# Performance work log

Hardware: AMD Instinct MI355X
Metric: run time of the kernel (lower is better)

The kernel has to match this reference:

```python
import jax, jax.numpy as jnp
import numpy as np

# Scattering config (matches init_kwargs)
T = 16384       # input_shape
J = 8           # max_scale_power
Q = 8           # fo_wavelets (first-order wavelets per octave); Q2 = 1
B = 16          # batch
STRIDE = 2 ** J # final lowpass subsampling -> output length T // STRIDE = 64
XI_MAX = 0.35   # max normalized center frequency (standard Morlet choice)


def _build_filters():
    """Analytic Morlet-style filter bank, defined directly in frequency domain
    as Gaussians (positive-frequency support -> analytic wavelets)."""
    freqs = np.arange(T, dtype=np.float64) / T  # normalized freq grid [0,1)
    # First order: Q wavelets per octave over J octaves
    n1 = J * Q
    xi1 = XI_MAX * 2.0 ** (-np.arange(n1) / Q)
    sigma1 = xi1 * (2.0 ** (1.0 / Q) - 1.0)          # bandwidth ~ filter spacing
    psi1 = np.exp(-(freqs[None, :] - xi1[:, None]) ** 2 / (2.0 * sigma1[:, None] ** 2))
    # Second order: Q2=1 wavelet per octave
    xi2 = XI_MAX * 2.0 ** (-np.arange(J, dtype=np.float64))
    sigma2 = xi2 * 0.5
    psi2 = np.exp(-(freqs[None, :] - xi2[:, None]) ** 2 / (2.0 * sigma2[:, None] ** 2))
    # Lowpass phi: Gaussian at DC with cutoff ~ 2^-J (symmetric in freq)
    f_sym = np.minimum(freqs, 1.0 - freqs)
    sigma_phi = XI_MAX * 2.0 ** (-J)
    phi = np.exp(-f_sym ** 2 / (2.0 * sigma_phi ** 2))
    # Valid second-order paths: xi2[j2] < xi1[j1] (frequency-decreasing cascade)
    i1g, i2g = np.meshgrid(np.arange(n1), np.arange(J), indexing="ij")
    valid = xi2[i2g] < xi1[i1g]
    pair_j1 = i1g[valid].astype(np.int32)  # 224 pairs for J=8, Q=8
    pair_j2 = i2g[valid].astype(np.int32)
    return (psi1.astype(np.float32), psi2.astype(np.float32),
            phi.astype(np.float32), pair_j1, pair_j2)


def setup_inputs() -> dict:
    key = jax.random.key(0)
    x = jax.random.normal(key, (B, T), dtype=jnp.float32)
    psi1, psi2, phi, p1, p2 = _build_filters()
    return {
        "x": x,
        "psi1_hat": jnp.asarray(psi1),   # [n1, T]
        "psi2_hat": jnp.asarray(psi2),   # [n2, T]
        "phi_hat": jnp.asarray(phi),     # [T]
        "pair_j1": jnp.asarray(p1),      # [P] int32
        "pair_j2": jnp.asarray(p2),      # [P] int32
    }


def reference(x, psi1_hat, psi2_hat, phi_hat, pair_j1, pair_j2):
    """1D wavelet scattering: FFT-domain Morlet convs + complex modulus +
    lowpass + downsample by 2^J. Returns (order0, order1, order2) coefficients,
    mirroring WaveletScatter1d's per-order tuple."""
    xh = jnp.fft.fft(x)                                             # [B, T] complex
    # Order 0: S0 = subsample(x * phi)
    S0 = jnp.fft.ifft(xh * phi_hat).real[:, None, ::STRIDE]          # [B, 1, T/2^J]
    # Order 1: U1_j = |x * psi1_j|
    U1 = jnp.abs(jnp.fft.ifft(xh[:, None, :] * psi1_hat[None, :, :]))  # [B, n1, T]
    U1h = jnp.fft.fft(U1)                                            # [B, n1, T]
    S1 = jnp.fft.ifft(U1h * phi_hat).real[:, :, ::STRIDE]            # [B, n1, T/2^J]
    # Order 2: U2_{j1,j2} = ||x*psi1_j1| * psi2_j2| for valid pairs (xi2 < xi1)
    U2 = jnp.abs(jnp.fft.ifft(U1h[:, pair_j1, :] * psi2_hat[pair_j2][None]))  # [B, P, T]
    S2 = jnp.fft.ifft(jnp.fft.fft(U2) * phi_hat).real[:, :, ::STRIDE]         # [B, P, T/2^J]
    return (S0, S1, S2)
```

## Files before the change

kernel.cpp:

```cpp
#include <hip/hip_runtime.h>
#include <math.h>


#define T_N   16384
#define NT    512
#define NTS   256
#define B_SZ  16
#define N1    64
#define NPAIR 224
#define FOLD_F 256
#define USTRIDE 8208
#define INV_N (1.0f/16384.0f)
#define TWO_PI 6.283185307179586f

typedef float v2f __attribute__((ext_vector_type(2)));

__device__ __forceinline__ int pad(int i) { return i + (i >> 4); }

__device__ __forceinline__ v2f cmulw(v2f a, v2f w){
  v2f n; n.x = -a.y; n.y = a.x;
  return w.x * a + w.y * n;
}
__device__ __forceinline__ constexpr int br4(int x){
  return ((x&1)<<3)|((x&2)<<1)|((x&4)>>1)|((x&8)>>3);
}
template<int LB>
__device__ __forceinline__ constexpr int brN(int x){
  int r=0;
  for(int i=0;i<LB;++i){ r=(r<<1)|((x>>i)&1); }
  return r;
}
__device__ __forceinline__ int rev4_14(int p){
  unsigned r = __brev((unsigned)p) >> 18;
  return (int)(((r & 0x2AAAu) >> 1) | ((r & 0x1555u) << 1));
}

__device__ __forceinline__ void twiddle_tree(v2f w, v2f* tw){
  tw[0].x = 1.f; tw[0].y = 0.f;
  tw[1] = w;
  tw[2] = cmulw(w, w);
  tw[4] = cmulw(tw[2], tw[2]);
  tw[8] = cmulw(tw[4], tw[4]);
  tw[3] = cmulw(tw[2], w);
  tw[5] = cmulw(tw[4], w);
  tw[6] = cmulw(tw[4], tw[2]);
  tw[7] = cmulw(tw[4], tw[3]);
  tw[9]  = cmulw(tw[8], w);
  tw[10] = cmulw(tw[8], tw[2]);
  tw[11] = cmulw(tw[8], tw[3]);
  tw[12] = cmulw(tw[8], tw[4]);
  tw[13] = cmulw(tw[8], tw[5]);
  tw[14] = cmulw(tw[8], tw[6]);
  tw[15] = cmulw(tw[8], tw[7]);
}

template<int SGN, int LOGNN>
__device__ __forceinline__ void dft_reg(v2f* a){
  constexpr int NN = 1<<LOGNN;
  static constexpr float C16[16] = {
    1.f, 0.98078528f, 0.92387953f, 0.83146961f, 0.70710678f, 0.55557023f,
    0.38268343f, 0.19509032f, 0.f, -0.19509032f, -0.38268343f, -0.55557023f,
    -0.70710678f, -0.83146961f, -0.92387953f, -0.98078528f };
  static constexpr float S16[16] = {
    0.f, 0.19509032f, 0.38268343f, 0.55557023f, 0.70710678f, 0.83146961f,
    0.92387953f, 0.98078528f, 1.f, 0.98078528f, 0.92387953f, 0.83146961f,
    0.70710678f, 0.55557023f, 0.38268343f, 0.19509032f };
#pragma unroll
  for (int m = NN/2; m >= 1; m >>= 1) {
#pragma unroll
    for (int base = 0; base < NN; base += 2*m) {
#pragma unroll
      for (int j = 0; j < m; ++j) {
        v2f u = a[base+j], v = a[base+j+m];
        a[base+j] = u + v;
        v2f w = u - v;
        const int ti = (j*16)/m;
        v2f tw; tw.x = C16[ti]; tw.y = (float)SGN * S16[ti];
        a[base+j+m] = cmulw(w, tw);
      }
    }
  }
}
template<int SGN>
__device__ __forceinline__ void dft16(v2f* a){ dft_reg<SGN,4>(a); }

template<int SGN, int M, int LOGM>
__device__ __forceinline__ void super_dif16(v2f* d, int g)
{
  const int j = g & (M-1);
  const int base = ((g >> LOGM) << (LOGM+4)) | j;
  v2f* dp = d + pad(base);
  v2f a[16];
#pragma unroll
  for (int k = 0; k < 16; ++k) a[k] = dp[k*M + ((k*M)>>4)];
  dft16<SGN>(a);
  float sj, cj;
  __sincosf((float)SGN * (TWO_PI / (16.f*(float)M)) * (float)j, &sj, &cj);
  v2f w; w.x = cj; w.y = sj;
  v2f tw[16];
  twiddle_tree(w, tw);
  dp[0] = a[0];
#pragma unroll
  for (int r = 1; r < 16; ++r)
    dp[r*M + ((r*M)>>4)] = cmulw(a[br4(r)], tw[r]);
}

template<int SGN, int M, int LOGM>
__device__ __forceinline__ void super_dif16_sp8(v2f* d, int g)
{
  static constexpr float CW[16] = { 1.f, 0.92387953f, 0.70710678f, 0.38268343f,
    0.f, -0.38268343f, -0.70710678f, -0.92387953f, -1.f, -0.92387953f,
    -0.70710678f, -0.38268343f, 0.f, 0.38268343f, 0.70710678f, 0.92387953f };
  static constexpr float SW[16] = { 0.f, 0.38268343f, 0.70710678f, 0.92387953f,
    1.f, 0.92387953f, 0.70710678f, 0.38268343f, 0.f, -0.38268343f,
    -0.70710678f, -0.92387953f, -1.f, -0.92387953f, -0.70710678f, -0.38268343f };
  const int j = g & (M-1);
  const int base = ((g >> LOGM) << (LOGM+4)) | j;
  v2f* dp = d + pad(base);
  v2f a[8];
#pragma unroll
  for (int m = 0; m < 8; ++m) a[m] = dp[m*M + ((m*M)>>4)];
  v2f y[16];
#pragma unroll
  for (int r0 = 0; r0 < 2; ++r0) {
    v2f z[8];
    z[0] = a[0];
#pragma unroll
    for (int m = 1; m < 8; ++m) {
      v2f w; w.x = CW[(m*r0)&15]; w.y = (float)SGN*SW[(m*r0)&15];
      z[m] = cmulw(a[m], w);
    }
    v2f E[4], O[4];
    {
      v2f e0=z[0]+z[4], e1=z[0]-z[4], o0=z[2]+z[6], o1=z[2]-z[6];
      v2f io; io.x=-(float)SGN*o1.y; io.y=(float)SGN*o1.x;
      E[0]=e0+o0; E[1]=e1+io; E[2]=e0-o0; E[3]=e1-io;
    }
    {
      v2f e0=z[1]+z[5], e1=z[1]-z[5], o0=z[3]+z[7], o1=z[3]-z[7];
      v2f io; io.x=-(float)SGN*o1.y; io.y=(float)SGN*o1.x;
      O[0]=e0+o0; O[1]=e1+io; O[2]=e0-o0; O[3]=e1-io;
    }
    constexpr float RT = 0.70710678f;
#pragma unroll
    for (int r1 = 0; r1 < 4; ++r1) {
      v2f w8;
      if (r1 == 0)      { w8.x = 1.f;  w8.y = 0.f; }
      else if (r1 == 1) { w8.x = RT;   w8.y = (float)SGN*RT; }
      else if (r1 == 2) { w8.x = 0.f;  w8.y = (float)SGN; }
      else              { w8.x = -RT;  w8.y = (float)SGN*RT; }
      v2f t = cmulw(O[r1], w8);
      y[2*r1 + r0]     = E[r1] + t;
      y[2*r1 + r0 + 8] = E[r1] - t;
    }
  }
  float sj, cj;
  __sincosf((float)SGN * (TWO_PI / (16.f*(float)M)) * (float)j, &sj, &cj);
  v2f w; w.x = cj; w.y = sj;
  v2f tw[16];
  twiddle_tree(w, tw);
  dp[0] = y[0];
#pragma unroll
  for (int r = 1; r < 16; ++r)
    dp[r*M + ((r*M)>>4)] = cmulw(y[r], tw[r]);
}

template<int SGN, int M, int LOGM>
__device__ __forceinline__ void super_dit16(v2f* d, int g)
{
  const int j = g & (M-1);
  const int base = ((g >> LOGM) << (LOGM+4)) | j;
  v2f* dp = d + pad(base);
  float sj, cj;
  __sincosf((float)SGN * (TWO_PI / (16.f*(float)M)) * (float)j, &sj, &cj);
  v2f w; w.x = cj; w.y = sj;
  v2f tw[16];
  twiddle_tree(w, tw);
  v2f a[16];
  a[0] = dp[0];
#pragma unroll
  for (int k = 1; k < 16; ++k)
    a[k] = cmulw(dp[k*M + ((k*M)>>4)], tw[k]);
  dft16<SGN>(a);
#pragma unroll
  for (int r = 0; r < 16; ++r) dp[r*M + ((r*M)>>4)] = a[br4(r)];
}

template<int SGN, int LOGM1, int RMAX, bool JLIM>
__device__ __forceinline__ void final_prune(v2f* ds, int t)
{
  static constexpr float CW[16] = { 1.f, 0.92387953f, 0.70710678f, 0.38268343f,
    0.f, -0.38268343f, -0.70710678f, -0.92387953f, -1.f, -0.92387953f,
    -0.70710678f, -0.38268343f, 0.f, 0.38268343f, 0.70710678f, 0.92387953f };
  static constexpr float SW[16] = { 0.f, 0.38268343f, 0.70710678f, 0.92387953f,
    1.f, 0.92387953f, 0.70710678f, 0.38268343f, 0.f, -0.38268343f,
    -0.70710678f, -0.92387953f, -1.f, -0.92387953f, -0.70710678f, -0.38268343f };
  constexpr int M1 = 1<<LOGM1;
  const int j = t;
  if (JLIM && j >= 256) return;
  v2f* dp = ds + j + (j>>4);
  float sj, cj;
  __sincosf((float)SGN * (TWO_PI / (16.f*(float)M1)) * (float)j, &sj, &cj);
  v2f w; w.x = cj; w.y = sj;
  v2f tw[16];
  twiddle_tree(w, tw);
  v2f b[16];
  b[0] = dp[0];
#pragma unroll
  for (int k = 1; k < 16; ++k)
    b[k] = cmulw(dp[k*M1 + ((k*M1)>>4)], tw[k]);
#pragma unroll
  for (int r = 0; r < RMAX; ++r) {
    v2f acc = b[0];
#pragma unroll
    for (int k = 1; k < 16; ++k) {
      v2f wc; wc.x = CW[(r*k)&15]; wc.y = (float)SGN*SW[(r*k)&15];
      acc += cmulw(b[k], wc);
    }
    dp[r*M1 + ((r*M1)>>4)] = acc;
  }
}

template<int SGN, int LOGM>
__device__ __forceinline__ void dif_chain(v2f* ds, int t){
  super_dif16<SGN, (1<<LOGM), LOGM>(ds, t);
  __syncthreads();
  if constexpr (LOGM > 4) dif_chain<SGN, LOGM-4>(ds, t);
}
template<int SGN, int LOGM, int LOGTOP>
__device__ __forceinline__ void dit_chain(v2f* ds, int t){
  super_dit16<SGN, (1<<LOGM), LOGM>(ds, t);
  __syncthreads();
  if constexpr (LOGM + 4 < LOGTOP) dit_chain<SGN, LOGM+4, LOGTOP>(ds, t);
}

template<int LOGMM>
__device__ __forceinline__ void mid_generic(v2f* ds, int t)
{
  constexpr int MM = 1<<LOGMM;
  v2f* dp = ds + 17*t;
#pragma unroll
  for (int q = 0; q < 16/MM; ++q) {
    v2f a[MM];
#pragma unroll
    for (int i = 0; i < MM; ++i) a[i] = dp[q*MM+i];
    dft_reg<+1,LOGMM>(a);
    v2f m[MM];
#pragma unroll
    for (int r = 0; r < MM; ++r) {
      v2f y = a[brN<LOGMM>(r)];
      m[r].x = INV_N * sqrtf(y.x*y.x + y.y*y.y);
      m[r].y = 0.f;
    }
    dft_reg<-1,LOGMM>(m);
#pragma unroll
    for (int k = 0; k < MM; ++k) dp[q*MM+k] = m[brN<LOGMM>(k)];
  }
}

template<int LOGN, int RMAX, bool JL, int K1ST>
__device__ __forceinline__ void o2_body(v2f* ds, int t)
{
  constexpr int LOGM1 = LOGN-4;
  if constexpr (K1ST == 16) super_dif16<+1, (1<<LOGM1), LOGM1>(ds, t);
  else                      super_dif16_sp8<+1, (1<<LOGM1), LOGM1>(ds, t);
  __syncthreads();
  dif_chain<+1, LOGM1-4>(ds, t);
  constexpr int LOGMM = ((LOGM1-5)%4)+1;
  mid_generic<LOGMM>(ds, t);
  __syncthreads();
  dit_chain<-1, LOGMM, LOGM1>(ds, t);
  final_prune<-1, LOGM1, RMAX, JL>(ds, t);
  __syncthreads();
}

template<int PERK>
__device__ __forceinline__ void fold_generic(const v2f* ds, const float* __restrict__ phi,
                                             float* outp, int t, float scale)
{
  const int k = t / PERK, g = t % PERK;
  float sv, cv, ss, cs;
  __sincosf((TWO_PI/64.f) * (float)((g*k) & 63), &sv, &cv);
  __sincosf((TWO_PI/64.f) * (float)((PERK*k) & 63), &ss, &cs);
  float acc = 0.f;
#pragma unroll
  for (int m = 0; m < 256/PERK; ++m) {
    const int f = g + PERK*m;
    v2f u = ds[f + (f>>4)];
    float wgt = phi[f] * ((f == 0) ? 1.f : 2.f);
    acc += wgt * (u.x*cv - u.y*sv);
    float nc = cv*cs - sv*ss, ns = cv*ss + sv*cs;
    cv = nc; sv = ns;
  }
#pragma unroll
  for (int o = 1; o < PERK; o <<= 1) acc += __shfl_xor(acc, o);
  if (g == 0) outp[k] = acc * scale;
}

__device__ __forceinline__ void fold32(v2f* ds, const float* __restrict__ phi,
                                       float* outp, int t, float scale, bool valid)
{
#pragma unroll
  for (int h = 0; h < 2; ++h) {
    const int g = t + 32*h;
    v2f acc; acc.x = 0.f; acc.y = 0.f;
#pragma unroll
    for (int m = 0; m < 4; ++m) {
      const int f = g + 64*m;
      v2f u = ds[f + (f>>4)];
      float wgt = phi[f] * ((f == 0) ? 1.f : 2.f);
      acc += wgt * u;
    }
    const int s = 384 + g;
    ds[s + (s>>4)] = acc;
  }
  __syncthreads();
  if (valid) {
#pragma unroll
    for (int h = 0; h < 2; ++h) {
      const int k = t + 32*h;
      float ss, cs;
      __sincosf((TWO_PI/64.f) * (float)k, &ss, &cs);
      float cv = 1.f, sv = 0.f, acc = 0.f;
      for (int g = 0; g < 64; ++g) {
        const int s = 384 + g;
        v2f V = ds[s + (s>>4)];
        acc += V.x*cv - V.y*sv;
        float nc = cv*cs - sv*ss, ns = cv*ss + sv*cs;
        cv = nc; sv = ns;
      }
      outp[k] = acc * scale;
    }
  }
}

__device__ __forceinline__ int pair_index(int j1, int j2)
{
  const int q = j1 >> 3;
  return 8*(7*q - (q*(q-1))/2) + (j1 & 7)*(7 - q) + (j2 - q - 1);
}

__device__ __constant__ int WTAB[8]  = {16384, 12903, 6452, 3226, 1613, 807, 404, 202};
__device__ __constant__ int TBTAB[8] = {4600, 2300, 1152, 576, 292, 148, 76, 40};

__device__ __forceinline__ float2 f2add(float2 a, float2 b){ return make_float2(a.x+b.x, a.y+b.y); }
__device__ __forceinline__ float2 f2sub(float2 a, float2 b){ return make_float2(a.x-b.x, a.y-b.y); }
__device__ __forceinline__ float2 cmul_cs(float2 a, float c, float s){
  return make_float2(a.x*c - a.y*s, a.x*s + a.y*c);
}
__device__ void dif_sweep(float2* d, int tid, float sgn, int mb_hi, int mb_lo)
{
  const float ang = sgn * (TWO_PI / (float)T_N);
  for (int mbits = mb_hi; mbits >= mb_lo; mbits -= 2) {
    const int M = 1 << mbits;
#pragma unroll 8
    for (int v = tid; v < T_N/4; v += NT) {
      const int j = v & (M-1);
      const int base = ((v >> mbits) << (mbits+2)) | j;
      const int i0 = pad(base), i1 = pad(base+M), i2 = pad(base+2*M), i3 = pad(base+3*M);
      float2 a0=d[i0], a1=d[i1], a2=d[i2], a3=d[i3];
      float2 t0=f2add(a0,a2), t1=f2sub(a0,a2), t2=f2add(a1,a3), t3=f2sub(a1,a3);
      float2 y0=f2add(t0,t2), y2=f2sub(t0,t2);
      float2 y1=make_float2(t1.x - sgn*t3.y, t1.y + sgn*t3.x);
      float2 y3=make_float2(t1.x + sgn*t3.y, t1.y - sgn*t3.x);
      float s1,c1;
      __sincosf(ang * (float)(j << (12-mbits)), &s1, &c1);
      float c2=c1*c1-s1*s1, s2=2.f*c1*s1;
      float c3=c1*c2-s1*s2, s3=c1*s2+s1*c2;
      d[i0]=y0;
      d[i1]=cmul_cs(y1,c1,s1);
      d[i2]=cmul_cs(y2,c2,s2);
      d[i3]=cmul_cs(y3,c3,s3);
    }
    __syncthreads();
  }
}
__device__ void fold_store8(const float2* d, const float* __restrict__ phi, float* outp, int tid)
{
  const int k = tid >> 3, g = tid & 7;
  float acc = 0.f;
  for (int f = g; f < FOLD_F; f += 8) {
    float2 u = d[pad(f)];
    float w = phi[f] * ((f == 0) ? 1.f : 2.f);
    float sv, cv;
    __sincosf((TWO_PI/64.f) * (float)((f*k) & 63), &sv, &cv);
    acc += w * (u.x*cv - u.y*sv);
  }
  acc += __shfl_xor(acc, 1);
  acc += __shfl_xor(acc, 2);
  acc += __shfl_xor(acc, 4);
  if (g == 0) outp[k] = acc * INV_N;
}

__global__ void __launch_bounds__(NT) k_fft_x(const float* __restrict__ x, const float* __restrict__ phi,
                                              float2* __restrict__ xh, float* __restrict__ out)
{
  extern __shared__ char smem[];
  float2* d = (float2*)smem;
  const int tid = threadIdx.x;
  const int b = blockIdx.x;
  const float* xr = x + b * T_N;
  for (int i = tid; i < T_N; i += NT) d[pad(i)] = make_float2(xr[i], 0.f);
  __syncthreads();
  dif_sweep(d, tid, -1.f, 12, 0);
  for (int p = tid; p < T_N; p += NT) {
    int r = rev4_14(p);
    if (p < r) { int ip = pad(p), ir = pad(r); float2 t = d[ip]; d[ip] = d[ir]; d[ir] = t; }
  }
  __syncthreads();
  float2* xrow = xh + (size_t)b * T_N;
  for (int i = tid; i < T_N; i += NT) xrow[i] = d[pad(i)];
  fold_store8(d, phi, out + b * 64, tid);
}

template<int LOGN>
__device__ __forceinline__ void o1_dec_body(v2f* sm, int sub, int t, int j1, int b,
    const float2* __restrict__ xh, const float* __restrict__ psi1,
    const float* __restrict__ phi, float2* __restrict__ u1h, float* __restrict__ out)
{
  constexpr int N = 1<<LOGN, SEGT = N/16;
  v2f* ds = sm + sub*N + ((sub*N)>>4);
  const float c = 5734.4f * exp2f(-0.125f*(float)j1);
  const int lo = max(0, (int)(0.36f*c));
  const int hi = min(T_N, (int)(1.64f*c)+2);
  const int W = hi - lo;
  const float2* xrow = xh + (size_t)b * T_N;
  const float* prow = psi1 + j1 * T_N;
#pragma unroll
  for (int s = 0; s < 16; ++s) {
    int f = t + s*SEGT;
    v2f z; z.x = 0.f; z.y = 0.f;
    if (f < W) { float2 xv = xrow[lo+f]; float p = prow[lo+f]; z.x = xv.x*p; z.y = xv.y*p; }
    ds[f + (f>>4)] = z;
  }
  __syncthreads();
  constexpr int RM = (LOGN == 9) ? 10 : 9;
  o2_body<LOGN, RM, false, 16>(ds, t);
  const int tb = TBTAB[(j1>>3) & 7];
  const float R = (float)(T_N >> LOGN);
  float2* urow = u1h + (size_t)(b*N1 + j1) * USTRIDE;
  for (int i = t; i < tb; i += SEGT) {
    v2f u = ds[i + (i>>4)];
    urow[i] = make_float2(R*u.x, R*u.y);
  }
  float* outp = out + 1024 + (size_t)(b*N1 + j1)*64;
  if constexpr (SEGT >= 64) fold_generic<SEGT/64>(ds, phi, outp, t, 1.f/(float)N);
  else                      fold32(ds, phi, outp, t, 1.f/(float)N, true);
}

__global__ void __launch_bounds__(NT, 4) k_o1a(const float2* __restrict__ xh, const float* __restrict__ psi1,
                                               const float* __restrict__ phi, float2* __restrict__ u1h,
                                               float* __restrict__ out)
{
  extern __shared__ char smem[];
  o1_dec_body<13>((v2f*)smem, 0, threadIdx.x, blockIdx.x / B_SZ, blockIdx.x % B_SZ,
                  xh, psi1, phi, u1h, out);
}

__global__ void __launch_bounds__(NTS, 4) k_o1b(const float2* __restrict__ xh, const float* __restrict__ psi1,
                                                const float* __restrict__ phi, float2* __restrict__ u1h,
                                                float* __restrict__ out)
{
  extern __shared__ char smem[];
  v2f* sm = (v2f*)smem;
  const int grp = blockIdx.x / B_SZ, b = blockIdx.x % B_SZ;
  const int tid = threadIdx.x;
  if (grp < 8) {
    o1_dec_body<12>(sm, 0, tid, 8 + grp, b, xh, psi1, phi, u1h, out);
  } else if (grp < 12) {
    const int sub = tid >> 7;
    o1_dec_body<11>(sm, sub, tid & 127, 16 + (grp-8)*2 + sub, b, xh, psi1, phi, u1h, out);
  } else if (grp < 14) {
    const int sub = tid >> 6;
    o1_dec_body<10>(sm, sub, tid & 63, 24 + (grp-12)*4 + sub, b, xh, psi1, phi, u1h, out);
  } else {
    const int sub = tid >> 5;
    o1_dec_body<9>(sm, sub, tid & 31, 32 + (grp-14)*8 + sub, b, xh, psi1, phi, u1h, out);
  }
}

template<int LOGN, int K1ST>
__device__ __forceinline__ void o2_cls_body(v2f* sm, int sub, int t, int b, int j1, int j2, bool valid,
    const float2* __restrict__ u1h, const float* __restrict__ psi2,
    const float* __restrict__ phi, float* __restrict__ out)
{
  constexpr int N = 1<<LOGN, SEGT = N/16;
  v2f* ds = sm + sub*N + ((sub*N)>>4);
  const int W  = WTAB[j2 & 7];
  const int tb = TBTAB[(j1 >> 3) & 7];
  const int lim = min(W, tb);
  const float2* urow = u1h + (size_t)(b * N1 + j1) * USTRIDE;
  const float* prow = psi2 + j2 * T_N;
#pragma unroll
  for (int s = 0; s < 16; ++s) {
    int f = t + s*SEGT;
    v2f z; z.x = 0.f; z.y = 0.f;
    if (valid && f < lim) { float2 u = urow[f]; float ps = prow[f]; z.x = u.x*ps; z.y = u.y*ps; }
    ds[f + (f>>4)] = z;
  }
  __syncthreads();
  constexpr int RM = ((1<<(LOGN-4)) >= 256) ? 1 : (256 >> (LOGN-4));
  constexpr bool JL = ((1<<(LOGN-4)) > 256);
  o2_body<LOGN, RM, JL, K1ST>(ds, t);
  float* outp = out + 66560 + (size_t)(b * NPAIR + pair_index(j1, j2)) * 64;
  if constexpr (SEGT >= 64) { if (valid) fold_generic<SEGT/64>(ds, phi, outp, t, 1.f/(float)N); }
  else                      fold32(ds, phi, outp, t, 1.f/(float)N, valid);
}

__global__ void __launch_bounds__(NT, 4) k_o2a(const float2* __restrict__ u1h, const float* __restrict__ psi2,
                                               const float* __restrict__ phi, float* __restrict__ out)
{
  extern __shared__ char smem[];
  const int grp = blockIdx.x / B_SZ, b = blockIdx.x % B_SZ;
  const int j2 = (grp < 8) ? 1 : 2;
  const int j1 = (grp < 8) ? grp : grp - 8;
  o2_cls_body<13,8>((v2f*)smem, 0, threadIdx.x, b, j1, j2, true, u1h, psi2, phi, out);
}

__global__ void __launch_bounds__(NTS, 4) k_o2b(const float2* __restrict__ u1h, const float* __restrict__ psi2,
                                                const float* __restrict__ phi, float* __restrict__ out)
{
  extern __shared__ char smem[];
  v2f* sm = (v2f*)smem;
  const int grp = blockIdx.x / B_SZ, b = blockIdx.x % B_SZ;
  const int tid = threadIdx.x;
  if (grp < 8) {
    o2_cls_body<12,16>(sm, 0, tid, b, 8 + grp, 2, true, u1h, psi2, phi, out);
  } else if (grp < 32) {
    o2_cls_body<12,16>(sm, 0, tid, b, grp - 8, 3, true, u1h, psi2, phi, out);
  } else if (grp < 48) {
    const int sub = tid >> 7;
    o2_cls_body<11,16>(sm, sub, tid & 127, b, (grp-32)*2 + sub, 4, true, u1h, psi2, phi, out);
  } else if (grp < 58) {
    const int sub = tid >> 6;
    o2_cls_body<10,16>(sm, sub, tid & 63, b, (grp-48)*4 + sub, 5, true, u1h, psi2, phi, out);
  } else if (grp < 64) {
    const int sub = tid >> 5;
    o2_cls_body<9,16>(sm, sub, tid & 31, b, (grp-58)*8 + sub, 6, true, u1h, psi2, phi, out);
  } else {
    const int sub = tid >> 5;
    o2_cls_body<9,8>(sm, sub, tid & 31, b, (grp-64)*8 + sub, 7, true, u1h, psi2, phi, out);
  }
}

extern "C" void kernel_launch(void* const* d_in, const int* in_sizes, int n_in,
                              void* d_out, int out_size, void* d_ws, size_t ws_size,
                              hipStream_t stream)
{
  const float* x    = (const float*)d_in[0];
  const float* psi1 = (const float*)d_in[1];
  const float* psi2 = (const float*)d_in[2];
  const float* phi  = (const float*)d_in[3];
  float* out = (float*)d_out;

  float2* xh  = (float2*)d_ws;
  float2* u1h = xh + (size_t)B_SZ * T_N;

  const size_t lds_h = (size_t)(T_N + (T_N >> 4)) * sizeof(float2);
  const size_t lds_l = (size_t)(8192 + (8192 >> 4)) * sizeof(float2);
  const size_t lds_s = (size_t)(4096 + (4096 >> 4)) * sizeof(float2);

  (void)hipFuncSetAttribute((const void*)k_fft_x, hipFuncAttributeMaxDynamicSharedMemorySize, (int)lds_h);
  (void)hipFuncSetAttribute((const void*)k_o1a,   hipFuncAttributeMaxDynamicSharedMemorySize, (int)lds_l);
  (void)hipFuncSetAttribute((const void*)k_o1b,   hipFuncAttributeMaxDynamicSharedMemorySize, (int)lds_s);
  (void)hipFuncSetAttribute((const void*)k_o2a,   hipFuncAttributeMaxDynamicSharedMemorySize, (int)lds_l);
  (void)hipFuncSetAttribute((const void*)k_o2b,   hipFuncAttributeMaxDynamicSharedMemorySize, (int)lds_s);

  hipLaunchKernelGGL(k_fft_x, dim3(B_SZ),      dim3(NT),  lds_h, stream, x, phi, xh, out);
  hipLaunchKernelGGL(k_o1a,   dim3(B_SZ * 8),  dim3(NT),  lds_l, stream, xh, psi1, phi, u1h, out);
  hipLaunchKernelGGL(k_o1b,   dim3(B_SZ * 18), dim3(NTS), lds_s, stream, xh, psi1, phi, u1h, out);
  hipLaunchKernelGGL(k_o2a,   dim3(B_SZ * 16), dim3(NT),  lds_l, stream, u1h, psi2, phi, out);
  hipLaunchKernelGGL(k_o2b,   dim3(B_SZ * 71), dim3(NTS), lds_s, stream, u1h, psi2, phi, out);
}
```

Measured before the change: 183.8 us.

## Resize FFT lengths per path and split small-FFT work into 128-thread kernels

Splits the first- and second-order launches into three size classes (512, 256 and 128 threads) so each wavelet path runs in a block sized to its decimated FFT length. Second-order paths with j2=2 now use 4096-point FFTs instead of 8192, and j2=4 paths use 2048-point FFTs, with the frequency-window limit clamped to N. Packing per block is rebalanced across more, smaller blocks. This is meant to cut wasted FFT work and raise occupancy, at the cost of one extra launch per stage and a possible accuracy change if the shorter transforms alias.

```diff
diff --git a/kernel.cpp b/kernel.cpp
--- a/kernel.cpp
+++ b/kernel.cpp
@@ -5,6 +5,7 @@
 #define T_N   16384
 #define NT    512
 #define NTS   256
+#define NTX   128
 #define B_SZ  16
 #define N1    64
 #define NPAIR 224
@@ -462,20 +463,26 @@
                                                 float* __restrict__ out)
 {
   extern __shared__ char smem[];
+  o1_dec_body<12>((v2f*)smem, 0, threadIdx.x, 8 + blockIdx.x / B_SZ, blockIdx.x % B_SZ,
+                  xh, psi1, phi, u1h, out);
+}
+
+__global__ void __launch_bounds__(NTX, 4) k_o1c(const float2* __restrict__ xh, const float* __restrict__ psi1,
+                                                const float* __restrict__ phi, float2* __restrict__ u1h,
+                                                float* __restrict__ out)
+{
+  extern __shared__ char smem[];
   v2f* sm = (v2f*)smem;
   const int grp = blockIdx.x / B_SZ, b = blockIdx.x % B_SZ;
   const int tid = threadIdx.x;
   if (grp < 8) {
-    o1_dec_body<12>(sm, 0, tid, 8 + grp, b, xh, psi1, phi, u1h, out);
+    o1_dec_body<11>(sm, 0, tid, 16 + grp, b, xh, psi1, phi, u1h, out);
   } else if (grp < 12) {
-    const int sub = tid >> 7;
-    o1_dec_body<11>(sm, sub, tid & 127, 16 + (grp-8)*2 + sub, b, xh, psi1, phi, u1h, out);
-  } else if (grp < 14) {
     const int sub = tid >> 6;
-    o1_dec_body<10>(sm, sub, tid & 63, 24 + (grp-12)*4 + sub, b, xh, psi1, phi, u1h, out);
+    o1_dec_body<10>(sm, sub, tid & 63, 24 + (grp-8)*2 + sub, b, xh, psi1, phi, u1h, out);
   } else {
     const int sub = tid >> 5;
-    o1_dec_body<9>(sm, sub, tid & 31, 32 + (grp-14)*8 + sub, b, xh, psi1, phi, u1h, out);
+    o1_dec_body<9>(sm, sub, tid & 31, 32 + (grp-12)*4 + sub, b, xh, psi1, phi, u1h, out);
   }
 }
 
@@ -488,7 +495,7 @@
   v2f* ds = sm + sub*N + ((sub*N)>>4);
   const int W  = WTAB[j2 & 7];
   const int tb = TBTAB[(j1 >> 3) & 7];
-  const int lim = min(W, tb);
+  const int lim = min(min(W, tb), N);
   const float2* urow = u1h + (size_t)(b * N1 + j1) * USTRIDE;
   const float* prow = psi2 + j2 * T_N;
 #pragma unroll
@@ -511,35 +518,41 @@
                                                const float* __restrict__ phi, float* __restrict__ out)
 {
   extern __shared__ char smem[];
+  o2_cls_body<13,8>((v2f*)smem, 0, threadIdx.x, blockIdx.x % B_SZ, blockIdx.x / B_SZ, 1, true,
+                    u1h, psi2, phi, out);
+}
+
+__global__ void __launch_bounds__(NTS, 4) k_o2b(const float2* __restrict__ u1h, const float* __restrict__ psi2,
+                                                const float* __restrict__ phi, float* __restrict__ out)
+{
+  extern __shared__ char smem[];
+  v2f* sm = (v2f*)smem;
   const int grp = blockIdx.x / B_SZ, b = blockIdx.x % B_SZ;
-  const int j2 = (grp < 8) ? 1 : 2;
-  const int j1 = (grp < 8) ? grp : grp - 8;
-  o2_cls_body<13,8>((v2f*)smem, 0, threadIdx.x, b, j1, j2, true, u1h, psi2, phi, out);
-}
-
-__global__ void __launch_bounds__(NTS, 4) k_o2b(const float2* __restrict__ u1h, const float* __restrict__ psi2,
+  if (grp < 16) {
+    o2_cls_body<12,16>(sm, 0, threadIdx.x, b, grp, 2, true, u1h, psi2, phi, out);
+  } else {
+    o2_cls_body<12,16>(sm, 0, threadIdx.x, b, grp - 16, 3, true, u1h, psi2, phi, out);
+  }
+}
+
+__global__ void __launch_bounds__(NTX, 4) k_o2c(const float2* __restrict__ u1h, const float* __restrict__ psi2,
                                                 const float* __restrict__ phi, float* __restrict__ out)
 {
   extern __shared__ char smem[];
   v2f* sm = (v2f*)smem;
   const int grp = blockIdx.x / B_SZ, b = blockIdx.x % B_SZ;
   const int tid = threadIdx.x;
-  if (grp < 8) {
-    o2_cls_body<12,16>(sm, 0, tid, b, 8 + grp, 2, true, u1h, psi2, phi, out);
-  } else if (grp < 32) {
-    o2_cls_body<12,16>(sm, 0, tid, b, grp - 8, 3, true, u1h, psi2, phi, out);
-  } else if (grp < 48) {
-    const int sub = tid >> 7;
-    o2_cls_body<11,16>(sm, sub, tid & 127, b, (grp-32)*2 + sub, 4, true, u1h, psi2, phi, out);
-  } else if (grp < 58) {
+  if (grp < 32) {
+    o2_cls_body<11,16>(sm, 0, tid, b, grp, 4, true, u1h, psi2, phi, out);
+  } else if (grp < 52) {
     const int sub = tid >> 6;
-    o2_cls_body<10,16>(sm, sub, tid & 63, b, (grp-48)*4 + sub, 5, true, u1h, psi2, phi, out);
+    o2_cls_body<10,16>(sm, sub, tid & 63, b, (grp-32)*2 + sub, 5, true, u1h, psi2, phi, out);
   } else if (grp < 64) {
     const int sub = tid >> 5;
-    o2_cls_body<9,16>(sm, sub, tid & 31, b, (grp-58)*8 + sub, 6, true, u1h, psi2, phi, out);
+    o2_cls_body<9,16>(sm, sub, tid & 31, b, (grp-52)*4 + sub, 6, true, u1h, psi2, phi, out);
   } else {
     const int sub = tid >> 5;
-    o2_cls_body<9,8>(sm, sub, tid & 31, b, (grp-64)*8 + sub, 7, true, u1h, psi2, phi, out);
+    o2_cls_body<9,8>(sm, sub, tid & 31, b, (grp-64)*4 + sub, 7, true, u1h, psi2, phi, out);
   }
 }
 
@@ -559,16 +572,21 @@
   const size_t lds_h = (size_t)(T_N + (T_N >> 4)) * sizeof(float2);
   const size_t lds_l = (size_t)(8192 + (8192 >> 4)) * sizeof(float2);
   const size_t lds_s = (size_t)(4096 + (4096 >> 4)) * sizeof(float2);
+  const size_t lds_x = (size_t)(2048 + (2048 >> 4)) * sizeof(float2);
 
   (void)hipFuncSetAttribute((const void*)k_fft_x, hipFuncAttributeMaxDynamicSharedMemorySize, (int)lds_h);
   (void)hipFuncSetAttribute((const void*)k_o1a,   hipFuncAttributeMaxDynamicSharedMemorySize, (int)lds_l);
   (void)hipFuncSetAttribute((const void*)k_o1b,   hipFuncAttributeMaxDynamicSharedMemorySize, (int)lds_s);
+  (void)hipFuncSetAttribute((const void*)k_o1c,   hipFuncAttributeMaxDynamicSharedMemorySize, (int)lds_x);
   (void)hipFuncSetAttribute((const void*)k_o2a,   hipFuncAttributeMaxDynamicSharedMemorySize, (int)lds_l);
   (void)hipFuncSetAttribute((const void*)k_o2b,   hipFuncAttributeMaxDynamicSharedMemorySize, (int)lds_s);
+  (void)hipFuncSetAttribute((const void*)k_o2c,   hipFuncAttributeMaxDynamicSharedMemorySize, (int)lds_x);
 
   hipLaunchKernelGGL(k_fft_x, dim3(B_SZ),      dim3(NT),  lds_h, stream, x, phi, xh, out);
   hipLaunchKernelGGL(k_o1a,   dim3(B_SZ * 8),  dim3(NT),  lds_l, stream, xh, psi1, phi, u1h, out);
-  hipLaunchKernelGGL(k_o1b,   dim3(B_SZ * 18), dim3(NTS), lds_s, stream, xh, psi1, phi, u1h, out);
-  hipLaunchKernelGGL(k_o2a,   dim3(B_SZ * 16), dim3(NT),  lds_l, stream, u1h, psi2, phi, out);
-  hipLaunchKernelGGL(k_o2b,   dim3(B_SZ * 71), dim3(NTS), lds_s, stream, u1h, psi2, phi, out);
-}
+  hipLaunchKernelGGL(k_o1b,   dim3(B_SZ * 8),  dim3(NTS), lds_s, stream, xh, psi1, phi, u1h, out);
+  hipLaunchKernelGGL(k_o1c,   dim3(B_SZ * 20), dim3(NTX), lds_x, stream, xh, psi1, phi, u1h, out);
+  hipLaunchKernelGGL(k_o2a,   dim3(B_SZ * 8),  dim3(NT),  lds_l, stream, u1h, psi2, phi, out);
+  hipLaunchKernelGGL(k_o2b,   dim3(B_SZ * 40), dim3(NTS), lds_s, stream, u1h, psi2, phi, out);
+  hipLaunchKernelGGL(k_o2c,   dim3(B_SZ * 78), dim3(NTX), lds_x, stream, u1h, psi2, phi, out);
+}
```

Measured after the change: 203.1 us. 10.5% more time.
